# Optimization experiments

Measured on AMD Instinct MI355X. Metric: run time of the kernel, lower is better.

The kernel has to match this reference:

```python
import jax, jax.numpy as jnp
import numpy as np

B, L = 16384, 32
IN_DIM, TIME_DIM, HIDDEN, HEADS = 128, 64, 256, 4
HEAD_DIM = HIDDEN // HEADS
KV_DIM = IN_DIM + 2 * TIME_DIM
EPS = 1e-5


def setup_inputs() -> dict:
    key = jax.random.key(0)
    ks = jax.random.split(key, 16)
    s = lambda d: 1.0 / np.sqrt(d)
    return {
        "x_u": jax.random.normal(ks[0], (B, IN_DIM), jnp.float32),
        "x_ctx": jax.random.normal(ks[1], (B, L, IN_DIM), jnp.float32),
        "t_ctx": jax.random.uniform(ks[2], (B, L), jnp.float32) * 100.0,
        "freq": jax.random.normal(ks[3], (TIME_DIM,), jnp.float32),
        "phase": jnp.zeros((TIME_DIM,), jnp.float32),
        "Wq": jax.random.normal(ks[4], (IN_DIM, HIDDEN), jnp.float32) * s(IN_DIM),
        "Wk": jax.random.normal(ks[5], (KV_DIM, HIDDEN), jnp.float32) * s(KV_DIM),
        "Wv": jax.random.normal(ks[6], (KV_DIM, HIDDEN), jnp.float32) * s(KV_DIM),
        "Wres": jax.random.normal(ks[7], (IN_DIM, HIDDEN), jnp.float32) * s(IN_DIM),
        "bres": jnp.zeros((HIDDEN,), jnp.float32),
        "W1": jax.random.normal(ks[8], (HIDDEN, HIDDEN), jnp.float32) * s(HIDDEN),
        "b1": jnp.zeros((HIDDEN,), jnp.float32),
        "W2": jax.random.normal(ks[9], (HIDDEN, HIDDEN), jnp.float32) * s(HIDDEN),
        "b2": jnp.zeros((HIDDEN,), jnp.float32),
        "g1": jnp.ones((HIDDEN,), jnp.float32),
        "be1": jnp.zeros((HIDDEN,), jnp.float32),
        "g2": jnp.ones((HIDDEN,), jnp.float32),
        "be2": jnp.zeros((HIDDEN,), jnp.float32),
    }


def _layernorm(x, g, b):
    m = jnp.mean(x, axis=-1, keepdims=True)
    v = jnp.mean((x - m) ** 2, axis=-1, keepdims=True)
    return (x - m) * jax.lax.rsqrt(v + EPS) * g + b


def reference(x_u, x_ctx, t_ctx, freq, phase, Wq, Wk, Wv, Wres, bres,
              W1, b1, W2, b2, g1, be1, g2, be2):
    # --- time encoding: [B, L, 2*TIME_DIM]
    z = jnp.log1p(jnp.maximum(t_ctx, 0.0))[..., None] * freq + phase
    te = jnp.concatenate([jnp.sin(z), jnp.cos(z)], axis=-1)

    # --- single-query multi-head attention over L neighbors
    q = (x_u @ Wq).reshape(B, HEADS, HEAD_DIM)            # [B,H,d]
    kv = jnp.concatenate([x_ctx, te], axis=-1)            # [B,L,KV_DIM]
    k = (kv @ Wk).reshape(B, L, HEADS, HEAD_DIM)          # [B,L,H,d]
    v = (kv @ Wv).reshape(B, L, HEADS, HEAD_DIM)
    att = jnp.einsum('bhd,blhd->bhl', q, k) / np.sqrt(HEAD_DIM)
    att = jax.nn.softmax(att, axis=-1)                    # [B,H,L]
    agg = jnp.einsum('bhl,blhd->bhd', att, v).reshape(B, HIDDEN)

    # --- residual + norms + FFN (dropout is identity in eval)
    z1 = _layernorm(agg + x_u @ Wres + bres, g1, be1)
    ff = jax.nn.relu(z1 @ W1 + b1) @ W2 + b2
    return _layernorm(ff + z1, g2, be2)
```

## Files before the change

### kernel.cpp

```cpp
#include <hip/hip_runtime.h>

typedef unsigned short u16;
typedef unsigned int   u32;

using bf16x8 = __attribute__((ext_vector_type(8))) short;
using f32x4  = __attribute__((ext_vector_type(4))) float;

#define MFMA16(A, B, C) __builtin_amdgcn_mfma_f32_16x16x32_bf16((A), (B), (C), 0, 0, 0)

static __device__ __forceinline__ u16 f2b(float f) {
    u32 u = __builtin_bit_cast(u32, f);
    u32 r = (u + 0x7FFFu + ((u >> 16) & 1u)) >> 16;
    return (u16)r;
}
static __device__ __forceinline__ bf16x8 cvt8(f32x4 a, f32x4 b) {
    bf16x8 r;
    r[0] = (short)f2b(a[0]); r[1] = (short)f2b(a[1]);
    r[2] = (short)f2b(a[2]); r[3] = (short)f2b(a[3]);
    r[4] = (short)f2b(b[0]); r[5] = (short)f2b(b[1]);
    r[6] = (short)f2b(b[2]); r[7] = (short)f2b(b[3]);
    return r;
}

__global__ __launch_bounds__(256) void k0_prep(
    const float* __restrict__ Wq, const float* __restrict__ Wk,
    const float* __restrict__ Wv, const float* __restrict__ Wres,
    const float* __restrict__ W1, const float* __restrict__ W2,
    u16* __restrict__ WcatT, u16* __restrict__ WresT,
    u16* __restrict__ WvT, u16* __restrict__ W1T, u16* __restrict__ W2T)
{
    int t = blockIdx.x * 256 + threadIdx.x;
    if (t < 131072) {
        int n = t >> 7, i = t & 127;
        int h = n >> 8, c = n & 255;
        const float* wq = Wq + i * 256 + h * 64;
        const float* wk = Wk + c * 256 + h * 64;
        float acc = 0.f;
        #pragma unroll 8
        for (int d = 0; d < 64; ++d) acc += wq[d] * wk[d];
        WcatT[t] = f2b(acc * 0.125f);
    } else if (t < 163840) {
        int o = t - 131072; int n = o >> 7, i = o & 127;
        WresT[o] = f2b(Wres[i * 256 + n]);
    } else if (t < 229376) {
        int o = t - 163840; int n = o >> 8, c = o & 255;
        WvT[o] = f2b(Wv[c * 256 + n]);
    } else if (t < 294912) {
        int o = t - 229376; int n = o >> 8, c = o & 255;
        W1T[o] = f2b(W1[c * 256 + n]);
    } else {
        int o = t - 294912; int n = o >> 8, c = o & 255;
        W2T[o] = f2b(W2[c * 256 + n]);
    }
}

__global__ __launch_bounds__(256) void k1_qkvec(
    const float* __restrict__ xu, const u16* __restrict__ WcatT,
    u16* __restrict__ qkvec)
{
    __shared__ __align__(16) u16 As[128][136];
    const int m0 = blockIdx.x * 128, n0 = blockIdx.y * 128;
    const int t = threadIdx.x;
    #pragma unroll
    for (int i = 0; i < 8; ++i) {
        int c = t + i * 256;
        int row = c >> 4, ch = c & 15;
        const float* src = xu + (size_t)(m0 + row) * 128 + ch * 8;
        f32x4 a = *(const f32x4*)src;
        f32x4 b = *(const f32x4*)(src + 4);
        *(bf16x8*)&As[row][ch * 8] = cvt8(a, b);
    }
    __syncthreads();
    const int lane = t & 63, wave = t >> 6;
    const int quad = lane >> 4, l16 = lane & 15;
    const int mh = (wave >> 1) * 64, nh = (wave & 1) * 64;
    f32x4 zz = {0.f, 0.f, 0.f, 0.f};
    f32x4 acc[4][4];
    #pragma unroll
    for (int mt = 0; mt < 4; ++mt)
        #pragma unroll
        for (int nt = 0; nt < 4; ++nt) acc[mt][nt] = zz;
    #pragma unroll
    for (int ks = 0; ks < 4; ++ks) {
        bf16x8 a[4], b[4];
        #pragma unroll
        for (int mt = 0; mt < 4; ++mt)
            a[mt] = *(const bf16x8*)&As[mh + mt * 16 + l16][ks * 32 + quad * 8];
        #pragma unroll
        for (int nt = 0; nt < 4; ++nt)
            b[nt] = *(const bf16x8*)(WcatT + (size_t)(n0 + nh + nt * 16 + l16) * 128 + ks * 32 + quad * 8);
        #pragma unroll
        for (int mt = 0; mt < 4; ++mt)
            #pragma unroll
            for (int nt = 0; nt < 4; ++nt)
                acc[mt][nt] = MFMA16(a[mt], b[nt], acc[mt][nt]);
    }
    #pragma unroll
    for (int mt = 0; mt < 4; ++mt)
        #pragma unroll
        for (int nt = 0; nt < 4; ++nt) {
            int col = n0 + nh + nt * 16 + l16;
            #pragma unroll
            for (int r = 0; r < 4; ++r) {
                int row = m0 + mh + mt * 16 + quad * 4 + r;
                qkvec[(size_t)row * 1024 + col] = f2b(acc[mt][nt][r]);
            }
        }
}

__global__ __launch_bounds__(256) void k2_attn(
    const float* __restrict__ x_ctx, const float* __restrict__ t_ctx,
    const float* __restrict__ freq, const float* __restrict__ phase,
    u16* __restrict__ qkv)
{
    __shared__ __align__(16) u16 kv_lc[32][264];
    __shared__ __align__(16) u16 kv_cl[256][40];
    __shared__ __align__(16) u16 pbuf[16][32];
    __shared__ float attbuf[32][5];
    __shared__ float lt[32];
    __shared__ float fr[64], ph[64];

    const int b = blockIdx.x;
    const int t = threadIdx.x;
    const int lane = t & 63, wave = t >> 6;
    const int quad = lane >> 4, l16 = lane & 15;

    if (t < 64) { fr[t] = freq[t]; ph[t] = phase[t]; }
    else if (t < 96) {
        int l = t - 64;
        lt[l] = log1pf(fmaxf(t_ctx[(size_t)b * 32 + l], 0.f));
    }
    ((u16*)pbuf)[t] = 0; ((u16*)pbuf)[t + 256] = 0;
    __syncthreads();

    if (t < 128) {
        #pragma unroll
        for (int i = 0; i < 4; ++i) {
            int idx = t + i * 128;
            int row = idx >> 4, ch = idx & 15;
            const float* src = x_ctx + (size_t)(b * 32 + row) * 128 + ch * 8;
            f32x4 a = *(const f32x4*)src;
            f32x4 bb = *(const f32x4*)(src + 4);
            bf16x8 vv = cvt8(a, bb);
            *(bf16x8*)&kv_lc[row][ch * 8] = vv;
            #pragma unroll
            for (int j = 0; j < 8; ++j)
                kv_cl[ch * 8 + j][row] = (u16)vv[j];
        }
    } else {
        int cc = t - 128;
        int f = cc & 63;
        float frq = fr[f], phs = ph[f];
        bool iscos = cc >= 64;
        for (int l = 0; l < 32; ++l) {
            float z = lt[l] * frq + phs;
            float v = iscos ? __cosf(z) : __sinf(z);
            u16 bv = f2b(v);
            kv_lc[l][128 + cc] = bv;
            kv_cl[128 + cc][l] = bv;
        }
    }
    __syncthreads();

    if (wave < 2) {
        f32x4 aacc = {0.f, 0.f, 0.f, 0.f};
        const u16* qb = qkv + (size_t)b * 1024 + (size_t)(l16 & 3) * 256;
        #pragma unroll
        for (int ks = 0; ks < 8; ++ks) {
            bf16x8 afr = *(const bf16x8*)&kv_lc[wave * 16 + l16][ks * 32 + quad * 8];
            bf16x8 bfr = *(const bf16x8*)(qb + ks * 32 + quad * 8);
            aacc = MFMA16(afr, bfr, aacc);
        }
        if (l16 < 4) {
            #pragma unroll
            for (int r = 0; r < 4; ++r)
                attbuf[wave * 16 + quad * 4 + r][l16] = aacc[r];
        }
    }
    __syncthreads();

    if (t < 128) {
        int h = t >> 5, l = t & 31;
        float a = attbuf[l][h];
        float m = a;
        #pragma unroll
        for (int s = 16; s > 0; s >>= 1) m = fmaxf(m, __shfl_xor(m, s));
        float p = __expf(a - m);
        float sum = p;
        #pragma unroll
        for (int s = 16; s > 0; s >>= 1) sum += __shfl_xor(sum, s);
        pbuf[h][l] = f2b(p / sum);
    }
    __syncthreads();

    {
        bf16x8 afr = *(const bf16x8*)&pbuf[l16][quad * 8];
        f32x4 zz = {0.f, 0.f, 0.f, 0.f};
        f32x4 cacc[4];
        #pragma unroll
        for (int nt = 0; nt < 4; ++nt) {
            bf16x8 bfr = *(const bf16x8*)&kv_cl[wave * 64 + nt * 16 + l16][quad * 8];
            cacc[nt] = MFMA16(afr, bfr, zz);
        }
        if (quad == 0) {
            #pragma unroll
            for (int nt = 0; nt < 4; ++nt) {
                int col = wave * 64 + nt * 16 + l16;
                #pragma unroll
                for (int r = 0; r < 4; ++r)
                    qkv[(size_t)b * 1024 + r * 256 + col] = f2b(cacc[nt][r]);
            }
        }
    }
}

__global__ __launch_bounds__(256) void k3_epilogue(
    const u16* __restrict__ ctxb, const float* __restrict__ xu,
    const u16* __restrict__ WvT, const u16* __restrict__ WresT,
    const u16* __restrict__ W1T, const u16* __restrict__ W2T,
    const float* __restrict__ bres, const float* __restrict__ b1,
    const float* __restrict__ b2, const float* __restrict__ g1,
    const float* __restrict__ be1, const float* __restrict__ g2,
    const float* __restrict__ be2, float* __restrict__ out)
{
    __shared__ __align__(16) char smem[39552];
    u16  (*ctxs)[1032] = reinterpret_cast<u16 (*)[1032]>(smem);
    u16  (*xus)[136]   = reinterpret_cast<u16 (*)[136]>(smem + 33024);
    float(*zbuf)[264]  = reinterpret_cast<float (*)[264]>(smem);
    u16  (*z1b)[264]   = reinterpret_cast<u16 (*)[264]>(smem + 16896);
    u16  (*h1b)[264]   = reinterpret_cast<u16 (*)[264]>(smem + 25344);
    float(*obuf)[264]  = reinterpret_cast<float (*)[264]>(smem + 16896);
    float(*red)[16][2] = reinterpret_cast<float (*)[16][2]>(smem + 37376);
    float(*mrstd)[2]   = reinterpret_cast<float (*)[2]>(smem + 39424);

    const int b0 = blockIdx.x * 16;
    const int t = threadIdx.x;
    const int lane = t & 63, wave = t >> 6;
    const int quad = lane >> 4, l16 = lane & 15;
    const int nw = wave * 64;

    #pragma unroll
    for (int i = 0; i < 8; ++i) {
        int idx = t + i * 256;
        int row = idx >> 7, ch = idx & 127;
        *(bf16x8*)&ctxs[row][ch * 8] = *(const bf16x8*)(ctxb + (size_t)(b0 + row) * 1024 + ch * 8);
    }
    {
        int row = t >> 4, ch = t & 15;
        const float* src = xu + (size_t)(b0 + row) * 128 + ch * 8;
        f32x4 a = *(const f32x4*)src;
        f32x4 b = *(const f32x4*)(src + 4);
        *(bf16x8*)&xus[row][ch * 8] = cvt8(a, b);
    }
    __syncthreads();

    f32x4 zz = {0.f, 0.f, 0.f, 0.f};

    f32x4 acc[4];
    #pragma unroll
    for (int nt = 0; nt < 4; ++nt) acc[nt] = zz;
    #pragma unroll
    for (int ks = 0; ks < 8; ++ks) {
        bf16x8 afr = *(const bf16x8*)&ctxs[l16][wave * 256 + ks * 32 + quad * 8];
        #pragma unroll
        for (int nt = 0; nt < 4; ++nt) {
            bf16x8 bfr = *(const bf16x8*)(WvT + (size_t)(nw + nt * 16 + l16) * 256 + ks * 32 + quad * 8);
            acc[nt] = MFMA16(afr, bfr, acc[nt]);
        }
    }
    #pragma unroll
    for (int ks = 0; ks < 4; ++ks) {
        bf16x8 afr = *(const bf16x8*)&xus[l16][ks * 32 + quad * 8];
        #pragma unroll
        for (int nt = 0; nt < 4; ++nt) {
            bf16x8 bfr = *(const bf16x8*)(WresT + (size_t)(nw + nt * 16 + l16) * 128 + ks * 32 + quad * 8);
            acc[nt] = MFMA16(afr, bfr, acc[nt]);
        }
    }
    __syncthreads();
    #pragma unroll
    for (int nt = 0; nt < 4; ++nt) {
        int col = nw + nt * 16 + l16;
        float bb = bres[col];
        #pragma unroll
        for (int r = 0; r < 4; ++r)
            zbuf[quad * 4 + r][col] = acc[nt][r] + bb;
    }
    __syncthreads();

    {
        int row = t >> 4, j = t & 15;
        float s = 0.f, s2 = 0.f;
        #pragma unroll
        for (int i = 0; i < 16; ++i) { float v = zbuf[row][j + 16 * i]; s += v; s2 += v * v; }
        red[row][j][0] = s; red[row][j][1] = s2;
    }
    __syncthreads();
    if (t < 16) {
        float s = 0.f, s2 = 0.f;
        #pragma unroll
        for (int j = 0; j < 16; ++j) { s += red[t][j][0]; s2 += red[t][j][1]; }
        float m = s * (1.f / 256.f);
        float var = s2 * (1.f / 256.f) - m * m;
        mrstd[t][0] = m;
        mrstd[t][1] = rsqrtf(var + 1e-5f);
    }
    __syncthreads();
    {
        float g = g1[t], be = be1[t];
        #pragma unroll
        for (int i = 0; i < 16; ++i) {
            float z = (zbuf[i][t] - mrstd[i][0]) * mrstd[i][1] * g + be;
            zbuf[i][t] = z;
            z1b[i][t] = f2b(z);
        }
    }
    __syncthreads();

    f32x4 acc2[4];
    #pragma unroll
    for (int nt = 0; nt < 4; ++nt) acc2[nt] = zz;
    #pragma unroll
    for (int ks = 0; ks < 8; ++ks) {
        bf16x8 afr = *(const bf16x8*)&z1b[l16][ks * 32 + quad * 8];
        #pragma unroll
        for (int nt = 0; nt < 4; ++nt) {
            bf16x8 bfr = *(const bf16x8*)(W1T + (size_t)(nw + nt * 16 + l16) * 256 + ks * 32 + quad * 8);
            acc2[nt] = MFMA16(afr, bfr, acc2[nt]);
        }
    }
    #pragma unroll
    for (int nt = 0; nt < 4; ++nt) {
        int col = nw + nt * 16 + l16;
        float bb = b1[col];
        #pragma unroll
        for (int r = 0; r < 4; ++r)
            h1b[quad * 4 + r][col] = f2b(fmaxf(acc2[nt][r] + bb, 0.f));
    }
    __syncthreads();

    f32x4 acc3[4];
    #pragma unroll
    for (int nt = 0; nt < 4; ++nt) acc3[nt] = zz;
    #pragma unroll
    for (int ks = 0; ks < 8; ++ks) {
        bf16x8 afr = *(const bf16x8*)&h1b[l16][ks * 32 + quad * 8];
        #pragma unroll
        for (int nt = 0; nt < 4; ++nt) {
            bf16x8 bfr = *(const bf16x8*)(W2T + (size_t)(nw + nt * 16 + l16) * 256 + ks * 32 + quad * 8);
            acc3[nt] = MFMA16(afr, bfr, acc3[nt]);
        }
    }
    __syncthreads();
    #pragma unroll
    for (int nt = 0; nt < 4; ++nt) {
        int col = nw + nt * 16 + l16;
        float bb = b2[col];
        #pragma unroll
        for (int r = 0; r < 4; ++r) {
            int row = quad * 4 + r;
            obuf[row][col] = acc3[nt][r] + bb + zbuf[row][col];
        }
    }
    __syncthreads();

    {
        int row = t >> 4, j = t & 15;
        float s = 0.f, s2 = 0.f;
        #pragma unroll
        for (int i = 0; i < 16; ++i) { float v = obuf[row][j + 16 * i]; s += v; s2 += v * v; }
        red[row][j][0] = s; red[row][j][1] = s2;
    }
    __syncthreads();
    if (t < 16) {
        float s = 0.f, s2 = 0.f;
        #pragma unroll
        for (int j = 0; j < 16; ++j) { s += red[t][j][0]; s2 += red[t][j][1]; }
        float m = s * (1.f / 256.f);
        float var = s2 * (1.f / 256.f) - m * m;
        mrstd[t][0] = m;
        mrstd[t][1] = rsqrtf(var + 1e-5f);
    }
    __syncthreads();
    {
        float g = g2[t], be = be2[t];
        #pragma unroll
        for (int i = 0; i < 16; ++i)
            out[(size_t)(b0 + i) * 256 + t] = (obuf[i][t] - mrstd[i][0]) * mrstd[i][1] * g + be;
    }
}

extern "C" void kernel_launch(void* const* d_in, const int* in_sizes, int n_in,
                              void* d_out, int out_size, void* d_ws, size_t ws_size,
                              hipStream_t stream)
{
    (void)in_sizes; (void)n_in; (void)out_size; (void)ws_size;
    const float* xu    = (const float*)d_in[0];
    const float* x_ctx = (const float*)d_in[1];
    const float* t_ctx = (const float*)d_in[2];
    const float* freq  = (const float*)d_in[3];
    const float* phase = (const float*)d_in[4];
    const float* Wq    = (const float*)d_in[5];
    const float* Wk    = (const float*)d_in[6];
    const float* Wv    = (const float*)d_in[7];
    const float* Wres  = (const float*)d_in[8];
    const float* bres  = (const float*)d_in[9];
    const float* W1    = (const float*)d_in[10];
    const float* b1    = (const float*)d_in[11];
    const float* W2    = (const float*)d_in[12];
    const float* b2    = (const float*)d_in[13];
    const float* g1    = (const float*)d_in[14];
    const float* be1   = (const float*)d_in[15];
    const float* g2    = (const float*)d_in[16];
    const float* be2   = (const float*)d_in[17];
    float* out = (float*)d_out;

    char* ws = (char*)d_ws;
    u16* qkv   = (u16*)(ws);
    u16* WcatT = (u16*)(ws + 33554432);
    u16* WresT = (u16*)(ws + 33816576);
    u16* WvT   = (u16*)(ws + 33882112);
    u16* W1T   = (u16*)(ws + 34013184);
    u16* W2T   = (u16*)(ws + 34144256);

    hipLaunchKernelGGL(k0_prep, dim3(1408), dim3(256), 0, stream,
                       Wq, Wk, Wv, Wres, W1, W2, WcatT, WresT, WvT, W1T, W2T);
    hipLaunchKernelGGL(k1_qkvec, dim3(128, 8), dim3(256), 0, stream,
                       xu, WcatT, qkv);
    hipLaunchKernelGGL(k2_attn, dim3(16384), dim3(256), 0, stream,
                       x_ctx, t_ctx, freq, phase, qkv);
    hipLaunchKernelGGL(k3_epilogue, dim3(1024), dim3(256), 0, stream,
                       qkv, xu, WvT, WresT, W1T, W2T,
                       bres, b1, b2, g1, be1, g2, be2, out);
}
```

Baseline: 504.7 us.

## Restructure attention kernel to one wave per batch row with register fragments

```diff
diff --git a/kernel.cpp b/kernel.cpp
--- a/kernel.cpp
+++ b/kernel.cpp
@@ -12,6 +12,21 @@
     u32 u = __builtin_bit_cast(u32, f);
     u32 r = (u + 0x7FFFu + ((u >> 16) & 1u)) >> 16;
     return (u16)r;
+}
+static __device__ __forceinline__ u16 f2bh(float f) {
+    u32 u = __builtin_bit_cast(u32, f) + 0x8000u;
+    return (u16)(u >> 16);
+}
+static __device__ __forceinline__ u32 pk2(float fa, float fb) {
+    u32 a = __builtin_bit_cast(u32, fa) + 0x8000u;
+    u32 b = __builtin_bit_cast(u32, fb) + 0x8000u;
+    return __builtin_amdgcn_perm(b, a, 0x07060302u);
+}
+static __device__ __forceinline__ bf16x8 cvt8f(f32x4 a, f32x4 b) {
+    union { u32 w[4]; bf16x8 v; } r;
+    r.w[0] = pk2(a[0], a[1]); r.w[1] = pk2(a[2], a[3]);
+    r.w[2] = pk2(b[0], b[1]); r.w[3] = pk2(b[2], b[3]);
+    return r.v;
 }
 static __device__ __forceinline__ bf16x8 cvt8(f32x4 a, f32x4 b) {
     bf16x8 r;
@@ -113,102 +128,126 @@
     const float* __restrict__ freq, const float* __restrict__ phase,
     u16* __restrict__ qkv)
 {
-    __shared__ __align__(16) u16 kv_lc[32][264];
-    __shared__ __align__(16) u16 kv_cl[256][40];
-    __shared__ __align__(16) u16 pbuf[16][32];
-    __shared__ float attbuf[32][5];
-    __shared__ float lt[32];
-    __shared__ float fr[64], ph[64];
-
-    const int b = blockIdx.x;
+    __shared__ __align__(16) u16 pw[4][4][32];
     const int t = threadIdx.x;
     const int lane = t & 63, wave = t >> 6;
     const int quad = lane >> 4, l16 = lane & 15;
-
-    if (t < 64) { fr[t] = freq[t]; ph[t] = phase[t]; }
-    else if (t < 96) {
-        int l = t - 64;
-        lt[l] = log1pf(fmaxf(t_ctx[(size_t)b * 32 + l], 0.f));
-    }
-    ((u16*)pbuf)[t] = 0; ((u16*)pbuf)[t + 256] = 0;
-    __syncthreads();
-
-    if (t < 128) {
-        #pragma unroll
-        for (int i = 0; i < 4; ++i) {
-            int idx = t + i * 128;
-            int row = idx >> 4, ch = idx & 15;
-            const float* src = x_ctx + (size_t)(b * 32 + row) * 128 + ch * 8;
-            f32x4 a = *(const f32x4*)src;
-            f32x4 bb = *(const f32x4*)(src + 4);
-            bf16x8 vv = cvt8(a, bb);
-            *(bf16x8*)&kv_lc[row][ch * 8] = vv;
-            #pragma unroll
-            for (int j = 0; j < 8; ++j)
-                kv_cl[ch * 8 + j][row] = (u16)vv[j];
-        }
-    } else {
-        int cc = t - 128;
-        int f = cc & 63;
-        float frq = fr[f], phs = ph[f];
-        bool iscos = cc >= 64;
-        for (int l = 0; l < 32; ++l) {
-            float z = lt[l] * frq + phs;
-            float v = iscos ? __cosf(z) : __sinf(z);
-            u16 bv = f2b(v);
-            kv_lc[l][128 + cc] = bv;
-            kv_cl[128 + cc][l] = bv;
-        }
-    }
-    __syncthreads();
-
-    if (wave < 2) {
-        f32x4 aacc = {0.f, 0.f, 0.f, 0.f};
-        const u16* qb = qkv + (size_t)b * 1024 + (size_t)(l16 & 3) * 256;
-        #pragma unroll
-        for (int ks = 0; ks < 8; ++ks) {
-            bf16x8 afr = *(const bf16x8*)&kv_lc[wave * 16 + l16][ks * 32 + quad * 8];
-            bf16x8 bfr = *(const bf16x8*)(qb + ks * 32 + quad * 8);
-            aacc = MFMA16(afr, bfr, aacc);
-        }
-        if (l16 < 4) {
+    const int b = blockIdx.x * 4 + wave;
+    const int fb = quad * 8;
+    const f32x4 zz = {0.f, 0.f, 0.f, 0.f};
+
+    float ltv = log1pf(fmaxf(t_ctx[(size_t)b * 32 + (lane & 31)], 0.f));
+
+    f32x4 fr0a = *(const f32x4*)(freq + fb);
+    f32x4 fr0b = *(const f32x4*)(freq + fb + 4);
+    f32x4 fr1a = *(const f32x4*)(freq + 32 + fb);
+    f32x4 fr1b = *(const f32x4*)(freq + 32 + fb + 4);
+    f32x4 ph0a = *(const f32x4*)(phase + fb);
+    f32x4 ph0b = *(const f32x4*)(phase + fb + 4);
+    f32x4 ph1a = *(const f32x4*)(phase + 32 + fb);
+    f32x4 ph1b = *(const f32x4*)(phase + 32 + fb + 4);
+
+    const u16* qb = qkv + (size_t)b * 1024 + (size_t)(l16 & 3) * 256;
+
+    f32x4 accA[2];
+    #pragma unroll
+    for (int ltile = 0; ltile < 2; ++ltile) {
+        const int l = ltile * 16 + l16;
+        const float* xrow = x_ctx + ((size_t)b * 32 + l) * 128;
+        f32x4 acc = zz;
+        #pragma unroll
+        for (int ks = 0; ks < 4; ++ks) {
+            f32x4 a = *(const f32x4*)(xrow + ks * 32 + fb);
+            f32x4 c = *(const f32x4*)(xrow + ks * 32 + fb + 4);
+            bf16x8 afr = cvt8f(a, c);
+            bf16x8 bfr = *(const bf16x8*)(qb + ks * 32 + fb);
+            acc = MFMA16(afr, bfr, acc);
+        }
+        float lt_l = __shfl(ltv, l);
+        f32x4 z0a = fr0a * lt_l + ph0a;
+        f32x4 z0b = fr0b * lt_l + ph0b;
+        f32x4 z1a = fr1a * lt_l + ph1a;
+        f32x4 z1b = fr1b * lt_l + ph1b;
+        f32x4 s0a, s0b, s1a, s1b, c0a, c0b, c1a, c1b;
+        #pragma unroll
+        for (int j = 0; j < 4; ++j) {
+            s0a[j] = __sinf(z0a[j]); s0b[j] = __sinf(z0b[j]);
+            s1a[j] = __sinf(z1a[j]); s1b[j] = __sinf(z1b[j]);
+            c0a[j] = __cosf(z0a[j]); c0b[j] = __cosf(z0b[j]);
+            c1a[j] = __cosf(z1a[j]); c1b[j] = __cosf(z1b[j]);
+        }
+        acc = MFMA16(cvt8f(s0a, s0b), *(const bf16x8*)(qb + 128 + fb), acc);
+        acc = MFMA16(cvt8f(s1a, s1b), *(const bf16x8*)(qb + 160 + fb), acc);
+        acc = MFMA16(cvt8f(c0a, c0b), *(const bf16x8*)(qb + 192 + fb), acc);
+        acc = MFMA16(cvt8f(c1a, c1b), *(const bf16x8*)(qb + 224 + fb), acc);
+        accA[ltile] = acc;
+    }
+
+    float m = accA[0][0];
+    #pragma unroll
+    for (int r = 1; r < 4; ++r) m = fmaxf(m, accA[0][r]);
+    #pragma unroll
+    for (int r = 0; r < 4; ++r) m = fmaxf(m, accA[1][r]);
+    m = fmaxf(m, __shfl_xor(m, 16));
+    m = fmaxf(m, __shfl_xor(m, 32));
+    float p[2][4], s = 0.f;
+    #pragma unroll
+    for (int lt2 = 0; lt2 < 2; ++lt2)
+        #pragma unroll
+        for (int r = 0; r < 4; ++r) { p[lt2][r] = __expf(accA[lt2][r] - m); s += p[lt2][r]; }
+    s += __shfl_xor(s, 16);
+    s += __shfl_xor(s, 32);
+    float inv = 1.f / s;
+    if (l16 < 4) {
+        #pragma unroll
+        for (int lt2 = 0; lt2 < 2; ++lt2)
             #pragma unroll
             for (int r = 0; r < 4; ++r)
-                attbuf[wave * 16 + quad * 4 + r][l16] = aacc[r];
-        }
-    }
-    __syncthreads();
-
-    if (t < 128) {
-        int h = t >> 5, l = t & 31;
-        float a = attbuf[l][h];
-        float m = a;
-        #pragma unroll
-        for (int s = 16; s > 0; s >>= 1) m = fmaxf(m, __shfl_xor(m, s));
-        float p = __expf(a - m);
-        float sum = p;
-        #pragma unroll
-        for (int s = 16; s > 0; s >>= 1) sum += __shfl_xor(sum, s);
-        pbuf[h][l] = f2b(p / sum);
-    }
-    __syncthreads();
-
-    {
-        bf16x8 afr = *(const bf16x8*)&pbuf[l16][quad * 8];
-        f32x4 zz = {0.f, 0.f, 0.f, 0.f};
-        f32x4 cacc[4];
-        #pragma unroll
-        for (int nt = 0; nt < 4; ++nt) {
-            bf16x8 bfr = *(const bf16x8*)&kv_cl[wave * 64 + nt * 16 + l16][quad * 8];
-            cacc[nt] = MFMA16(afr, bfr, zz);
-        }
+                pw[wave][l16][lt2 * 16 + quad * 4 + r] = f2bh(p[lt2][r] * inv);
+    }
+    __syncthreads();
+
+    bf16x8 pfr = *(const bf16x8*)&pw[wave][l16 & 3][fb];
+    float ltj[8];
+    #pragma unroll
+    for (int j = 0; j < 8; ++j) ltj[j] = __shfl(ltv, fb + j);
+
+    u16* crow = qkv + (size_t)b * 1024;
+    #pragma unroll
+    for (int nt = 0; nt < 8; ++nt) {
+        int c = nt * 16 + l16;
+        const float* xp = x_ctx + ((size_t)b * 32 + fb) * 128 + c;
+        float v0 = xp[0], v1 = xp[128], v2 = xp[256], v3 = xp[384];
+        float v4 = xp[512], v5 = xp[640], v6 = xp[768], v7 = xp[896];
+        union { u32 w[4]; bf16x8 v; } bu;
+        bu.w[0] = pk2(v0, v1); bu.w[1] = pk2(v2, v3);
+        bu.w[2] = pk2(v4, v5); bu.w[3] = pk2(v6, v7);
+        f32x4 d = MFMA16(pfr, bu.v, zz);
         if (quad == 0) {
             #pragma unroll
-            for (int nt = 0; nt < 4; ++nt) {
-                int col = wave * 64 + nt * 16 + l16;
-                #pragma unroll
-                for (int r = 0; r < 4; ++r)
-                    qkv[(size_t)b * 1024 + r * 256 + col] = f2b(cacc[nt][r]);
+            for (int r = 0; r < 4; ++r) crow[r * 256 + c] = f2bh(d[r]);
+        }
+    }
+    #pragma unroll
+    for (int pp = 0; pp < 4; ++pp) {
+        int f = pp * 16 + l16;
+        float fq = freq[f], phf = phase[f];
+        float z8[8];
+        #pragma unroll
+        for (int j = 0; j < 8; ++j) z8[j] = ltj[j] * fq + phf;
+        union { u32 w[4]; bf16x8 v; } bs, bc;
+        #pragma unroll
+        for (int j = 0; j < 4; ++j) {
+            bs.w[j] = pk2(__sinf(z8[2 * j]), __sinf(z8[2 * j + 1]));
+            bc.w[j] = pk2(__cosf(z8[2 * j]), __cosf(z8[2 * j + 1]));
+        }
+        f32x4 ds = MFMA16(pfr, bs.v, zz);
+        f32x4 dc = MFMA16(pfr, bc.v, zz);
+        if (quad == 0) {
+            #pragma unroll
+            for (int r = 0; r < 4; ++r) {
+                crow[r * 256 + 128 + f] = f2bh(ds[r]);
+                crow[r * 256 + 192 + f] = f2bh(dc[r]);
             }
         }
     }
@@ -427,7 +466,7 @@
                        Wq, Wk, Wv, Wres, W1, W2, WcatT, WresT, WvT, W1T, W2T);
     hipLaunchKernelGGL(k1_qkvec, dim3(128, 8), dim3(256), 0, stream,
                        xu, WcatT, qkv);
-    hipLaunchKernelGGL(k2_attn, dim3(16384), dim3(256), 0, stream,
+    hipLaunchKernelGGL(k2_attn, dim3(4096), dim3(256), 0, stream,
                        x_ctx, t_ctx, freq, phase, qkv);
     hipLaunchKernelGGL(k3_epilogue, dim3(1024), dim3(256), 0, stream,
                        qkv, xu, WvT, WresT, W1T, W2T,
```

After: 502.9 us. No clear change (-0.4%).
